# Optimization experiments

Hardware: AMD Instinct MI355X
Metric: run time of the kernel (lower is better)

## Reference

```python
import jax, jax.numpy as jnp
import numpy as np

N_NODES = 200000
N_EDGES = 440000
N_GRAPHS = 4096
EMB = 300
N_LAYERS = 5
TEMP = 0.04
NUM_ATOM_TYPE, NUM_CHIRALITY = 120, 3
NUM_BOND_TYPE, NUM_BOND_DIR = 6, 3
SELF_LOOP_TYPE = 4  # pretrain-gnns convention: self-loop edge_attr = [4, 0]


def setup_inputs() -> dict:
    key = jax.random.key(0)
    ks = jax.random.split(key, 24)
    inp = {}
    for i in (0, 1):
        inp[f"x{i}"] = jax.random.randint(ks[i * 4 + 0], (N_NODES, 2), 0, 3)
        inp[f"edge_index{i}"] = jax.random.randint(ks[i * 4 + 1], (2, N_EDGES), 0, N_NODES)
        inp[f"edge_attr{i}"] = jax.random.randint(ks[i * 4 + 2], (N_EDGES, 2), 0, 3)
        inp[f"batch_ids{i}"] = jnp.sort(jax.random.randint(ks[i * 4 + 3], (N_NODES,), 0, N_GRAPHS))

    def rn(k, shape, s=0.1):
        return (jax.random.normal(k, shape, jnp.float32) * s)

    inp["atom_emb1"] = rn(ks[8], (NUM_ATOM_TYPE, EMB))
    inp["atom_emb2"] = rn(ks[9], (NUM_CHIRALITY, EMB))
    inp["edge_emb1"] = rn(ks[10], (N_LAYERS, NUM_BOND_TYPE, EMB))
    inp["edge_emb2"] = rn(ks[11], (N_LAYERS, NUM_BOND_DIR, EMB))
    inp["W1"] = rn(ks[12], (N_LAYERS, EMB, 2 * EMB))
    inp["bm1"] = jnp.zeros((N_LAYERS, 2 * EMB), jnp.float32)
    inp["W2"] = rn(ks[13], (N_LAYERS, 2 * EMB, EMB))
    inp["bm2"] = jnp.zeros((N_LAYERS, EMB), jnp.float32)
    inp["gamma"] = jnp.ones((N_LAYERS, EMB), jnp.float32)
    inp["beta"] = jnp.zeros((N_LAYERS, EMB), jnp.float32)
    inp["Wp1"] = rn(ks[14], (EMB, EMB))
    inp["bp1"] = jnp.zeros((EMB,), jnp.float32)
    inp["Wp2"] = rn(ks[15], (EMB, EMB))
    inp["bp2"] = jnp.zeros((EMB,), jnp.float32)
    return inp


def _encode(x, edge_index, edge_attr, batch_ids,
            atom_emb1, atom_emb2, edge_emb1, edge_emb2,
            W1, bm1, W2, bm2, gamma, beta, Wp1, bp1, Wp2, bp2):
    n = x.shape[0]
    src, dst = edge_index[0], edge_index[1]
    h = atom_emb1[x[:, 0]] + atom_emb2[x[:, 1]]  # [N, EMB]
    for l in range(N_LAYERS):
        e = edge_emb1[l][edge_attr[:, 0]] + edge_emb2[l][edge_attr[:, 1]]  # [E, EMB]
        self_e = edge_emb1[l][SELF_LOOP_TYPE] + edge_emb2[l][0]  # self-loop edge emb
        # GIN sum aggregation (incl. self-loop message h_i + self_e)
        agg = jax.ops.segment_sum(h[src] + e, dst, num_segments=n) + h + self_e
        h = jax.nn.relu(agg @ W1[l] + bm1[l]) @ W2[l] + bm2[l]
        # BatchNorm over nodes (training-mode statistics, eps=1e-5)
        mean = h.mean(axis=0)
        var = h.var(axis=0)
        h = (h - mean) * jax.lax.rsqrt(var + 1e-5) * gamma[l] + beta[l]
        if l < N_LAYERS - 1:
            h = jax.nn.relu(h)
    # global_mean_pool
    s = jax.ops.segment_sum(h, batch_ids, num_segments=N_GRAPHS)
    c = jax.ops.segment_sum(jnp.ones((n, 1), h.dtype), batch_ids, num_segments=N_GRAPHS)
    g = s / jnp.maximum(c, 1.0)
    out = jax.nn.relu(g @ Wp1 + bp1) @ Wp2 + bp2
    return out / jnp.linalg.norm(out, axis=1, keepdims=True)


def reference(x0, edge_index0, edge_attr0, batch_ids0,
              x1, edge_index1, edge_attr1, batch_ids1,
              atom_emb1, atom_emb2, edge_emb1, edge_emb2,
              W1, bm1, W2, bm2, gamma, beta, Wp1, bp1, Wp2, bp2):
    params = (atom_emb1, atom_emb2, edge_emb1, edge_emb2,
              W1, bm1, W2, bm2, gamma, beta, Wp1, bp1, Wp2, bp2)
    f0 = _encode(x0, edge_index0, edge_attr0, batch_ids0, *params)
    f1 = _encode(x1, edge_index1, edge_attr1, batch_ids1, *params)
    logits = (f0 @ f1.T) / TEMP
    labels = jnp.arange(logits.shape[0])
    return logits, labels
```

## Files before the change

kernel.cpp:

```cpp
#include <hip/hip_runtime.h>
#include <hip/hip_bf16.h>
#include <hip/hip_fp16.h>

#define EMB 300
#define NHID 600
#define NLAYERS 5
#define NG 4096
#define NCOMBO 18
#define SELFCB 12
#define HS 304
#define KP1 320
#define KP2 640
#define SCB 2048

__device__ __forceinline__ void atomAddF(float* p, float v) { unsafeAtomicAdd(p, v); }

struct f8 { unsigned char v; };

__device__ __forceinline__ unsigned char enc8(float x) {
    unsigned xb = __float_as_uint(x);
    unsigned s = (xb >> 24) & 0x80u;
    float a = __uint_as_float(xb & 0x7FFFFFFFu);
    if (!(a < 448.f)) return (unsigned char)(s | 0x7E);
    if (a < 0.0009765625f) return (unsigned char)s;
    if (a < 0.015625f) {
        int m = (int)(a * 512.f + 0.5f);
        if (m > 7) return (unsigned char)(s | 0x08);
        return (unsigned char)(s | (unsigned)m);
    }
    unsigned u = __float_as_uint(a) + 0x80000u;
    int e = (int)(u >> 23) - 127;
    if (e > 8) return (unsigned char)(s | 0x7E);
    unsigned m = (u >> 20) & 7u;
    return (unsigned char)(s | ((unsigned)(e + 7) << 3) | m);
}
__device__ __forceinline__ float dec8(unsigned char c) {
    unsigned s = c & 0x80u, e = (c >> 3) & 0xFu, m = c & 7u;
    float v = (e == 0) ? (float)m * 0.001953125f
                       : __uint_as_float(((e + 120u) << 23) | (m << 20));
    return s ? -v : v;
}

typedef float fx2 __attribute__((ext_vector_type(2)));

#if defined(__has_builtin)
#if __has_builtin(__builtin_amdgcn_cvt_pk_f32_fp8) && __has_builtin(__builtin_amdgcn_cvt_pk_fp8_f32)
#define HWFP8 1
#endif
#endif

__device__ __forceinline__ void dec4(unsigned w, float& v0, float& v1, float& v2, float& v3) {
#ifdef HWFP8
    fx2 lo = __builtin_amdgcn_cvt_pk_f32_fp8((int)w, false);
    fx2 hi = __builtin_amdgcn_cvt_pk_f32_fp8((int)w, true);
    v0 = lo.x; v1 = lo.y; v2 = hi.x; v3 = hi.y;
#else
    v0 = dec8(w & 0xff); v1 = dec8((w >> 8) & 0xff);
    v2 = dec8((w >> 16) & 0xff); v3 = dec8((w >> 24) & 0xff);
#endif
}
__device__ __forceinline__ unsigned enc4(float v0, float v1, float v2, float v3) {
#ifdef HWFP8
    int w = __builtin_amdgcn_cvt_pk_fp8_f32(v0, v1, 0, false);
    w = __builtin_amdgcn_cvt_pk_fp8_f32(v2, v3, w, true);
    return (unsigned)w;
#else
    return (unsigned)enc8(v0) | ((unsigned)enc8(v1) << 8)
         | ((unsigned)enc8(v2) << 16) | ((unsigned)enc8(v3) << 24);
#endif
}
__device__ __forceinline__ unsigned char enc1(float v) {
#ifdef HWFP8
    return (unsigned char)(__builtin_amdgcn_cvt_pk_fp8_f32(v, 0.f, 0, false) & 0xff);
#else
    return enc8(v);
#endif
}
__device__ __forceinline__ float dec1(unsigned char c) {
#ifdef HWFP8
    fx2 lo = __builtin_amdgcn_cvt_pk_f32_fp8((int)(unsigned)c, false);
    return lo.x;
#else
    return dec8(c);
#endif
}

typedef _Float16 f16t;
typedef _Float16 f16x8 __attribute__((ext_vector_type(8)));
typedef float f32x4 __attribute__((ext_vector_type(4)));

__device__ __forceinline__ void stF(float* p, float v) { *p = v; }
__device__ __forceinline__ void stF(__half* p, float v) { *p = __float2half(v); }


__global__ void zero_f32_v6(float* __restrict__ p, long n) {
    long s = (long)gridDim.x * blockDim.x;
    for (long i = blockIdx.x * (long)blockDim.x + threadIdx.x; i < n; i += s) p[i] = 0.f;
}
__global__ void zero_i32_v8(int* __restrict__ p, int n) {
    int s = gridDim.x * blockDim.x;
    for (int i = blockIdx.x * blockDim.x + threadIdx.x; i < n; i += s) p[i] = 0;
}
__global__ void copy_i32_v8(const int* __restrict__ a, int* __restrict__ b, int n) {
    int s = gridDim.x * blockDim.x;
    for (int i = blockIdx.x * blockDim.x + threadIdx.x; i < n; i += s) b[i] = a[i];
}
__global__ void labels_v6(float* __restrict__ out, int n) {
    int i = blockIdx.x * blockDim.x + threadIdx.x;
    if (i < n) out[i] = (float)i;
}


__global__ void hist_dst_v8(const int* __restrict__ ei, int* __restrict__ deg, int E) {
    int s = gridDim.x * blockDim.x;
    for (int e = blockIdx.x * blockDim.x + threadIdx.x; e < E; e += s)
        atomicAdd(&deg[ei[E + e]], 1);
}
__global__ void hist_b_v8(const int* __restrict__ b, int* __restrict__ deg, int n) {
    int s = gridDim.x * blockDim.x;
    for (int i = blockIdx.x * blockDim.x + threadIdx.x; i < n; i += s)
        atomicAdd(&deg[b[i]], 1);
}

__global__ __launch_bounds__(256) void scan_excl_v8(const int* __restrict__ in,
                                                    int* __restrict__ out, int n) {
    __shared__ int part[256];
    int span = (n + 255) / 256;
    int t = threadIdx.x;
    int s0 = t * span, s1 = min(s0 + span, n);
    int sum = 0;
    for (int i = s0; i < s1; ++i) sum += in[i];
    part[t] = sum;
    __syncthreads();
    int v = sum;
    for (int off = 1; off < 256; off <<= 1) {
        int u = (t >= off) ? part[t - off] : 0;
        __syncthreads();
        part[t] += u;
        __syncthreads();
    }
    int run = part[t] - v;
    for (int i = s0; i < s1; ++i) { out[i] = run; run += in[i]; }
    if (t == 255) out[n] = run;
}

__global__ __launch_bounds__(256) void scan_bsum_v10(const int* __restrict__ in,
                                                     int* __restrict__ bsum, int n) {
    __shared__ int red[256];
    int b = blockIdx.x, t = threadIdx.x;
    int base = b * SCB + t * 8;
    int s = 0;
#pragma unroll
    for (int i = 0; i < 8; ++i) { int idx = base + i; if (idx < n) s += in[idx]; }
    red[t] = s; __syncthreads();
#pragma unroll
    for (int o = 128; o > 0; o >>= 1) {
        if (t < o) red[t] += red[t + o];
        __syncthreads();
    }
    if (t == 0) bsum[b] = red[0];
}

__global__ __launch_bounds__(256) void scan_top_v10(int* __restrict__ bsum, int nb,
                                                    int* __restrict__ total_out) {
    __shared__ int part[256];
    int t = threadIdx.x;
    int v = (t < nb) ? bsum[t] : 0;
    part[t] = v;
    __syncthreads();
    for (int o = 1; o < 256; o <<= 1) {
        int u = (t >= o) ? part[t - o] : 0;
        __syncthreads();
        part[t] += u;
        __syncthreads();
    }
    if (t < nb) bsum[t] = part[t] - v;
    if (t == 255) *total_out = part[255];
}

__global__ __launch_bounds__(256) void scan_fill_v10(const int* __restrict__ in,
                                                     const int* __restrict__ bsum,
                                                     int* __restrict__ out, int n) {
    __shared__ int red[256];
    int b = blockIdx.x, t = threadIdx.x;
    int base = b * SCB + t * 8;
    int v[8]; int s = 0;
#pragma unroll
    for (int i = 0; i < 8; ++i) { int idx = base + i; v[i] = (idx < n) ? in[idx] : 0; s += v[i]; }
    red[t] = s;
    __syncthreads();
    int self = s;
    for (int o = 1; o < 256; o <<= 1) {
        int u = (t >= o) ? red[t - o] : 0;
        __syncthreads();
        red[t] += u;
        __syncthreads();
    }
    int run = bsum[b] + red[t] - self;
#pragma unroll
    for (int i = 0; i < 8; ++i) { int idx = base + i; if (idx < n) out[idx] = run; run += v[i]; }
}

__global__ void fill_csr_v8(const int* __restrict__ ei, const int* __restrict__ ea,
                            int* __restrict__ cursor, int* __restrict__ csrc,
                            int* __restrict__ ccombo, int E) {
    int s = gridDim.x * blockDim.x;
    for (int e = blockIdx.x * blockDim.x + threadIdx.x; e < E; e += s) {
        int dst = ei[E + e];
        int pos = atomicAdd(&cursor[dst], 1);
        csrc[pos] = ei[e];
        ccombo[pos] = ea[2 * e] * 3 + ea[2 * e + 1];
    }
}

__global__ void tbl_v8(const float* __restrict__ ee1, const float* __restrict__ ee2,
                       float* __restrict__ tbl) {
    int idx = blockIdx.x * blockDim.x + threadIdx.x;
    if (idx >= NLAYERS * NCOMBO * EMB) return;
    int j = idx % EMB;
    int cb = (idx / EMB) % NCOMBO;
    int l = idx / (EMB * NCOMBO);
    tbl[idx] = ee1[(l * 6 + cb / 3) * EMB + j] + ee2[(l * 3 + cb % 3) * EMB + j];
}

__global__ void wtrans_v9(const float* __restrict__ W, f16t* __restrict__ Wt,
                          int K, int N, int Kpad) {
    int idx = blockIdx.x * blockDim.x + threadIdx.x;
    if (idx >= N * Kpad) return;
    int n = idx / Kpad, k = idx - n * Kpad;
    Wt[idx] = (k < K) ? (f16t)W[(size_t)k * N + n] : (f16t)0.f;
}

__global__ void wtrans8_v13(const float* __restrict__ W, unsigned char* __restrict__ Wt,
                            int K, int N, int Kpad) {
    int idx = blockIdx.x * blockDim.x + threadIdx.x;
    if (idx >= N * Kpad) return;
    int n = idx / Kpad, k = idx - n * Kpad;
    Wt[idx] = (k < K) ? enc8(W[(size_t)k * N + n]) : 0;
}


__global__ void init_h_v11(const int* __restrict__ x, const float* __restrict__ ae1,
                           const float* __restrict__ ae2, unsigned char* __restrict__ h,
                           int N) {
    int s = gridDim.x * blockDim.x;
    int total = N * (HS / 4);
    for (int idx = blockIdx.x * blockDim.x + threadIdx.x; idx < total; idx += s) {
        int i = idx / (HS / 4), d = idx - i * (HS / 4);
        int j = d * 4;
        int x0 = x[2 * i] * EMB, x1 = x[2 * i + 1] * EMB;
        unsigned out = 0;
#pragma unroll
        for (int t = 0; t < 4; ++t) {
            int jj = j + t;
            unsigned char b = 0;
            if (jj < EMB) b = enc8(ae1[x0 + jj] + ae2[x1 + jj]);
            out |= (unsigned)b << (8 * t);
        }
        *(unsigned*)(h + (size_t)i * HS + j) = out;
    }
}

template<bool BN>
__global__ __launch_bounds__(256)
void gather_v18(const unsigned char* __restrict__ h, const int* __restrict__ rp,
                const int* __restrict__ csrc, const int* __restrict__ ccombo,
                const float* __restrict__ tbl, const float* __restrict__ scl,
                const float* __restrict__ sft, unsigned char* __restrict__ aggc,
                int c0, int c1) {
    __shared__ float T[NCOMBO * EMB];
    __shared__ float SC[EMB + 4];
    __shared__ float SF[EMB + 4];
    for (int t = threadIdx.x; t < NCOMBO * EMB; t += 256) T[t] = tbl[t];
    if (BN) {
        for (int t = threadIdx.x; t < EMB; t += 256) { SC[t] = scl[t]; SF[t] = sft[t]; }
    }
    __syncthreads();
    int wid = (blockIdx.x * blockDim.x + threadIdx.x) >> 6;
    int lane = threadIdx.x & 63;
    int nw = (gridDim.x * blockDim.x) >> 6;
    const int jt = 256 + lane;
    float4 sc4, sf4; float sct = 1.f, sff = 0.f;
    if (BN) {
        sc4 = *(const float4*)&SC[lane << 2];
        sf4 = *(const float4*)&SF[lane << 2];
        if (lane < 44) { sct = SC[jt]; sff = SF[jt]; }
    }
#define BNAPP(val, sc, sf) { if (BN) (val) = fmaxf(fmaf((val), (sc), (sf)), 0.f); }
    for (int i = c0 + wid; i < c1; i += nw) {
        int p0 = rp[i], p1 = rp[i + 1];
        float a0, a1, a2, a3, at = 0.f;
        {
            const unsigned char* hr = h + (size_t)i * HS;
            unsigned w = *(const unsigned*)(hr + (lane << 2));
            float4 t4 = *(const float4*)&T[SELFCB * EMB + (lane << 2)];
            float v0, v1, v2, v3;
            dec4(w, v0, v1, v2, v3);
            BNAPP(v0, sc4.x, sf4.x); BNAPP(v1, sc4.y, sf4.y);
            BNAPP(v2, sc4.z, sf4.z); BNAPP(v3, sc4.w, sf4.w);
            a0 = v0 + t4.x; a1 = v1 + t4.y; a2 = v2 + t4.z; a3 = v3 + t4.w;
            if (lane < 44) {
                float vt = dec1(hr[jt]);
                BNAPP(vt, sct, sff);
                at = vt + T[SELFCB * EMB + jt];
            }
        }
        int p = p0;
        for (; p + 1 < p1; p += 2) {
            int sA = csrc[p],     cbA = ccombo[p];
            int sB = csrc[p + 1], cbB = ccombo[p + 1];
            const unsigned char* hA = h + (size_t)sA * HS;
            const unsigned char* hB = h + (size_t)sB * HS;
            unsigned wA = *(const unsigned*)(hA + (lane << 2));
            unsigned wB = *(const unsigned*)(hB + (lane << 2));
            float tA = 0.f, tB = 0.f;
            if (lane < 44) { tA = dec1(hA[jt]); tB = dec1(hB[jt]); }
            {
                float4 t4 = *(const float4*)&T[cbA * EMB + (lane << 2)];
                float v0, v1, v2, v3;
                dec4(wA, v0, v1, v2, v3);
                BNAPP(v0, sc4.x, sf4.x); BNAPP(v1, sc4.y, sf4.y);
                BNAPP(v2, sc4.z, sf4.z); BNAPP(v3, sc4.w, sf4.w);
                a0 += v0 + t4.x; a1 += v1 + t4.y; a2 += v2 + t4.z; a3 += v3 + t4.w;
                if (lane < 44) {
                    BNAPP(tA, sct, sff);
                    at += tA + T[cbA * EMB + jt];
                }
            }
            {
                float4 t4 = *(const float4*)&T[cbB * EMB + (lane << 2)];
                float v0, v1, v2, v3;
                dec4(wB, v0, v1, v2, v3);
                BNAPP(v0, sc4.x, sf4.x); BNAPP(v1, sc4.y, sf4.y);
                BNAPP(v2, sc4.z, sf4.z); BNAPP(v3, sc4.w, sf4.w);
                a0 += v0 + t4.x; a1 += v1 + t4.y; a2 += v2 + t4.z; a3 += v3 + t4.w;
                if (lane < 44) {
                    BNAPP(tB, sct, sff);
                    at += tB + T[cbB * EMB + jt];
                }
            }
        }
        if (p < p1) {
            int sA = csrc[p], cbA = ccombo[p];
            const unsigned char* hA = h + (size_t)sA * HS;
            unsigned wA = *(const unsigned*)(hA + (lane << 2));
            float4 t4 = *(const float4*)&T[cbA * EMB + (lane << 2)];
            float v0, v1, v2, v3;
            dec4(wA, v0, v1, v2, v3);
            BNAPP(v0, sc4.x, sf4.x); BNAPP(v1, sc4.y, sf4.y);
            BNAPP(v2, sc4.z, sf4.z); BNAPP(v3, sc4.w, sf4.w);
            a0 += v0 + t4.x; a1 += v1 + t4.y; a2 += v2 + t4.z; a3 += v3 + t4.w;
            if (lane < 44) {
                float vt = dec1(hA[jt]);
                BNAPP(vt, sct, sff);
                at += vt + T[cbA * EMB + jt];
            }
        }
        unsigned char* out = aggc + (size_t)(i - c0) * KP1;
        *(unsigned*)(out + (lane << 2)) = enc4(a0, a1, a2, a3);
        if (lane < 44) out[jt] = enc1(at);
    }
#undef BNAPP
}

template<int MODE, bool STATS>
__global__ __launch_bounds__(256)
void fast_gemm8_v16(const unsigned char* __restrict__ A, int lda,
                    const unsigned char* __restrict__ Bt, int ldb,
                    const float* __restrict__ bias, unsigned char* __restrict__ C,
                    int ldc, int M, int N, int Kpad, int gx,
                    float* __restrict__ sums)
{
    __shared__ char smem[26624];
    char* AlB = smem;
    char* BlB = smem + 9216;
    const int tid = threadIdx.x;
    const int lane = tid & 63;
    const int wid = tid >> 6;
    const int wr = (wid >> 1) << 6;
    const int wc = (wid & 1) << 6;

    const int nwg = gridDim.x;
    const int q = nwg >> 3, r = nwg & 7;
    const int xcd = blockIdx.x & 7, idx = blockIdx.x >> 3;
    const int swz = (xcd < r ? xcd * (q + 1) : r * (q + 1) + (xcd - r) * q) + idx;
    const int row0 = (swz / gx) * 128;
    const int col0 = (swz % gx) * 128;

    f32x4 acc[4][4] = {};
    const int nkt = Kpad >> 6;
    const int sr = tid >> 1;
    const int skb = (tid & 1) << 5;

    for (int kt = 0; kt < nkt; ++kt) {
        const int k0 = kt << 6;
        {
            const int gr = row0 + sr;
            const unsigned char* src = A + (size_t)gr * lda + k0 + skb;
            int4 v0 = {0, 0, 0, 0}, v1 = {0, 0, 0, 0};
            if (gr < M) { v0 = *(const int4*)src; v1 = *(const int4*)(src + 16); }
            char* dst = AlB + sr * 72 + skb;
            *(long*)(dst)      = ((const long*)&v0)[0];
            *(long*)(dst + 8)  = ((const long*)&v0)[1];
            *(long*)(dst + 16) = ((const long*)&v1)[0];
            *(long*)(dst + 24) = ((const long*)&v1)[1];
        }
        {
            const int gc = col0 + sr;
            const unsigned char* src = Bt + (size_t)gc * ldb + k0 + skb;
            int4 v0 = {0, 0, 0, 0}, v1 = {0, 0, 0, 0};
            if (gc < N) { v0 = *(const int4*)src; v1 = *(const int4*)(src + 16); }
            char* dst = BlB + sr * 72 + skb;
            *(long*)(dst)      = ((const long*)&v0)[0];
            *(long*)(dst + 8)  = ((const long*)&v0)[1];
            *(long*)(dst + 16) = ((const long*)&v1)[0];
            *(long*)(dst + 24) = ((const long*)&v1)[1];
        }
        __syncthreads();
        const int fr = lane & 15;
        const int kbase = (lane >> 4) << 3;
#pragma unroll
        for (int ks = 0; ks < 2; ++ks) {
            const int kg = kbase + ks * 32;
            long af[4], bf[4];
#pragma unroll
            for (int mi = 0; mi < 4; ++mi)
                af[mi] = *(const long*)(AlB + (wr + mi * 16 + fr) * 72 + kg);
#pragma unroll
            for (int ni = 0; ni < 4; ++ni)
                bf[ni] = *(const long*)(BlB + (wc + ni * 16 + fr) * 72 + kg);
#pragma unroll
            for (int mi = 0; mi < 4; ++mi)
#pragma unroll
                for (int ni = 0; ni < 4; ++ni)
                    acc[mi][ni] = __builtin_amdgcn_mfma_f32_16x16x32_fp8_fp8(
                        af[mi], bf[ni], acc[mi][ni], 0, 0, 0);
        }
        __syncthreads();
    }
    char* Cl = smem;
    float* Sred = (float*)(smem + 18432);
    float* Qred = (float*)(smem + 22528);
    const int fr = lane & 15;
    const int rb = (lane >> 4) << 2;
    const int slot = ((wid >> 1) << 2) | (lane >> 4);
#pragma unroll
    for (int ni = 0; ni < 4; ++ni) {
        const int cb = wc + ni * 16 + fr;
        const int c = col0 + cb;
        const float bv = (c < N) ? bias[c] : 0.f;
        float lsum = 0.f, lsq = 0.f;
#pragma unroll
        for (int mi = 0; mi < 4; ++mi) {
#pragma unroll
            for (int i = 0; i < 4; ++i) {
                const int rloc = wr + mi * 16 + rb + i;
                float v = acc[mi][ni][i] + bv;
                if (MODE == 2) v = fmaxf(v, 0.f);
                Cl[rloc * 144 + cb] = (char)enc1(v);
                if (STATS && (row0 + rloc) < M && c < N) {
                    lsum += v; lsq = fmaf(v, v, lsq);
                }
            }
        }
        if (STATS) { Sred[cb * 8 + slot] = lsum; Qred[cb * 8 + slot] = lsq; }
    }
    __syncthreads();
    {
        const int rloc = tid >> 1;
        const int half = (tid & 1) << 6;
        const int grow = row0 + rloc;
        if (grow < M) {
            int cmax = ldc - col0; if (cmax > 128) cmax = 128;
            unsigned char* dst = C + (size_t)grow * ldc + col0;
            const char* srcl = Cl + rloc * 144 + half;
#pragma unroll
            for (int qi = 0; qi < 4; ++qi) {
                if (half + qi * 16 + 16 <= cmax)
                    *(int4*)(dst + half + qi * 16) = *(const int4*)(srcl + qi * 16);
            }
        }
    }
    if (STATS) {
        if (tid < 128) {
            const int c = col0 + tid;
            if (c < N) {
                float s = 0.f, qq = 0.f;
#pragma unroll
                for (int k = 0; k < 8; ++k) { s += Sred[tid * 8 + k]; qq += Qred[tid * 8 + k]; }
                atomAddF(&sums[c], s);
                atomAddF(&sums[EMB + c], qq);
            }
        }
    }
}

template<typename TO, int MODE>
__global__ __launch_bounds__(256)
void fast_gemm_v12(const f16t* __restrict__ A, int lda,
                   const f16t* __restrict__ Bt, int ldb,
                   const float* __restrict__ bias, TO* __restrict__ C, int ldc,
                   int M, int N, int Kpad, float scale)
{
    __shared__ f16t Al[128][76];
    __shared__ f16t Bl[128][76];
    const int tid = threadIdx.x;
    const int lane = tid & 63;
    const int wid = tid >> 6;
    const int wr = (wid >> 1) << 6;
    const int wc = (wid & 1) << 6;
    const int row0 = blockIdx.y * 128;
    const int col0 = blockIdx.x * 128;
    f32x4 acc[4][4] = {};
    const int nkt = Kpad >> 6;
    const int sr = tid >> 1;
    const int skb = (tid & 1) << 5;

    for (int kt = 0; kt < nkt; ++kt) {
        const int k0 = kt << 6;
        {
            const int gr = row0 + sr;
            const f16t* src = A + (size_t)gr * lda + k0 + skb;
            f16x8 v0 = {}, v1 = {}, v2 = {}, v3 = {};
            if (gr < M) {
                v0 = *(const f16x8*)(src);
                v1 = *(const f16x8*)(src + 8);
                v2 = *(const f16x8*)(src + 16);
                v3 = *(const f16x8*)(src + 24);
            }
            *(f16x8*)&Al[sr][skb]      = v0;
            *(f16x8*)&Al[sr][skb + 8]  = v1;
            *(f16x8*)&Al[sr][skb + 16] = v2;
            *(f16x8*)&Al[sr][skb + 24] = v3;
        }
        {
            const int gc = col0 + sr;
            const f16t* src = Bt + (size_t)gc * ldb + k0 + skb;
            f16x8 v0 = {}, v1 = {}, v2 = {}, v3 = {};
            if (gc < N) {
                v0 = *(const f16x8*)(src);
                v1 = *(const f16x8*)(src + 8);
                v2 = *(const f16x8*)(src + 16);
                v3 = *(const f16x8*)(src + 24);
            }
            *(f16x8*)&Bl[sr][skb]      = v0;
            *(f16x8*)&Bl[sr][skb + 8]  = v1;
            *(f16x8*)&Bl[sr][skb + 16] = v2;
            *(f16x8*)&Bl[sr][skb + 24] = v3;
        }
        __syncthreads();
        const int fr = lane & 15;
        const int kbase = (lane >> 4) << 3;
#pragma unroll
        for (int ks = 0; ks < 2; ++ks) {
            const int kg8 = kbase + ks * 32;
            f16x8 af[4], bf[4];
#pragma unroll
            for (int mi = 0; mi < 4; ++mi)
                af[mi] = *(const f16x8*)&Al[wr + mi * 16 + fr][kg8];
#pragma unroll
            for (int ni = 0; ni < 4; ++ni)
                bf[ni] = *(const f16x8*)&Bl[wc + ni * 16 + fr][kg8];
#pragma unroll
            for (int mi = 0; mi < 4; ++mi)
#pragma unroll
                for (int ni = 0; ni < 4; ++ni)
                    acc[mi][ni] = __builtin_amdgcn_mfma_f32_16x16x32_f16(
                        af[mi], bf[ni], acc[mi][ni], 0, 0, 0);
        }
        __syncthreads();
    }
    const int fr = lane & 15;
    const int rb = (lane >> 4) << 2;
#pragma unroll
    for (int ni = 0; ni < 4; ++ni) {
        const int c = col0 + wc + ni * 16 + fr;
        if (c >= N) continue;
        const float bv = (MODE == 1 || MODE == 2) ? bias[c] : 0.f;
#pragma unroll
        for (int mi = 0; mi < 4; ++mi) {
#pragma unroll
            for (int i = 0; i < 4; ++i) {
                const int r = row0 + wr + mi * 16 + rb + i;
                if (r >= M) continue;
                float v = acc[mi][ni][i];
                if (MODE == 1 || MODE == 2) v += bv;
                if (MODE == 2) v = fmaxf(v, 0.f);
                v *= scale;
                if (MODE == 3) v = fmaxf(-26.f, fminf(26.f, v));
                stF(&C[(size_t)r * ldc + c], v);
            }
        }
    }
}


__global__ void bn_finalize_v6(const float* __restrict__ sums,
                               const float* __restrict__ gamma, const float* __restrict__ beta,
                               float* __restrict__ scl, float* __restrict__ sft, float inv_n) {
    int j = threadIdx.x;
    if (j < EMB) {
        float m = sums[j] * inv_n;
        float var = sums[EMB + j] * inv_n - m * m;
        float sc = gamma[j] * rsqrtf(var + 1e-5f);
        scl[j] = sc;
        sft[j] = beta[j] - m * sc;
    }
}


__global__ __launch_bounds__(256) void pool_seg_v11(const unsigned char* __restrict__ h,
                                                    const int* __restrict__ gptr,
                                                    const float* __restrict__ scl,
                                                    const float* __restrict__ sft,
                                                    __half* __restrict__ poolh) {
    int g = blockIdx.x;
    int s0 = gptr[g], s1 = gptr[g + 1];
    float inv = (s1 > s0) ? 1.f / (float)(s1 - s0) : 0.f;
    for (int j = threadIdx.x; j < EMB; j += 256) {
        float s = 0.f;
        for (int r = s0; r < s1; ++r) s += dec1(h[(size_t)r * HS + j]);
        float mv = (s1 > s0) ? fmaf(s * inv, scl[j], sft[j]) : 0.f;
        poolh[(size_t)g * KP1 + j] = __float2half(mv);
    }
}


__global__ __launch_bounds__(256) void rownorm_f16_v12(const float* __restrict__ f,
                                                       f16t* __restrict__ fh) {
    __shared__ float red[256];
    __shared__ float inv;
    int r = blockIdx.x, tid = threadIdx.x;
    const float* row = f + (size_t)r * EMB;
    float s = 0.f;
    for (int j = tid; j < EMB; j += 256) { float v = row[j]; s = fmaf(v, v, s); }
    red[tid] = s;
    __syncthreads();
#pragma unroll
    for (int o = 128; o > 0; o >>= 1) {
        if (tid < o) red[tid] += red[tid + o];
        __syncthreads();
    }
    if (tid == 0) inv = rsqrtf(fmaxf(red[0], 1e-30f));
    __syncthreads();
    float iv = inv;
    for (int j = tid; j < KP1; j += 256)
        fh[(size_t)r * KP1 + j] = (j < EMB) ? (f16t)(row[j] * iv) : (f16t)0.f;
}


extern "C" void kernel_launch(void* const* d_in, const int* in_sizes, int n_in,
                              void* d_out, int out_size, void* d_ws, size_t ws_size,
                              hipStream_t stream) {
    const int N = in_sizes[0] / 2;
    const int E = in_sizes[1] / 2;

    const float* atom1 = (const float*)d_in[8];
    const float* atom2 = (const float*)d_in[9];
    const float* ee1   = (const float*)d_in[10];
    const float* ee2   = (const float*)d_in[11];
    const float* W1    = (const float*)d_in[12];
    const float* bm1   = (const float*)d_in[13];
    const float* W2    = (const float*)d_in[14];
    const float* bm2   = (const float*)d_in[15];
    const float* gamma = (const float*)d_in[16];
    const float* beta  = (const float*)d_in[17];
    const float* Wp1   = (const float*)d_in[18];
    const float* bp1   = (const float*)d_in[19];
    const float* Wp2   = (const float*)d_in[20];
    const float* bp2   = (const float*)d_in[21];

    float* ob = (float*)d_out;

    unsigned char* h0 = (unsigned char*)d_out;
    bool h0_fits = ((size_t)N * HS) <= ((size_t)NG * NG * 4 - 256);

    size_t off = 0;
    char* base = (char*)d_ws;
    auto take = [&](size_t bytes) -> char* {
        char* p = base + off;
        off += (bytes + 255) & ~(size_t)255;
        return p;
    };
    unsigned char* h1 = (unsigned char*)take((size_t)N * HS);
    float* fbuf   = (float*)take((size_t)NG * EMB * 4);
    f16t*  fh     = (f16t*)take((size_t)2 * NG * KP1 * 2);
    float* sums   = (float*)take(2 * EMB * 4);
    float* scl    = (float*)take((size_t)NLAYERS * EMB * 4);
    float* sft    = (float*)take((size_t)NLAYERS * EMB * 4);
    int*   deg    = (int*)take((size_t)N * 4);
    int*   rp     = (int*)take((size_t)(N + 1) * 4);
    int*   cursor = (int*)take((size_t)N * 4);
    int*   csrc   = (int*)take((size_t)E * 4);
    int*   ccombo = (int*)take((size_t)E * 4);
    int*   bsum   = (int*)take(256 * 4);
    int*   gdeg   = (int*)take((size_t)NG * 4);
    int*   gptr   = (int*)take((size_t)(NG + 1) * 4);
    float* tbl    = (float*)take((size_t)NLAYERS * NCOMBO * EMB * 4);
    unsigned char* W1t8 = (unsigned char*)take((size_t)NLAYERS * NHID * KP1);
    unsigned char* W2t8 = (unsigned char*)take((size_t)NLAYERS * EMB * KP2);
    f16t*  Wp1t   = (f16t*)take((size_t)EMB * KP1 * 2);
    f16t*  Wp2t   = (f16t*)take((size_t)EMB * KP1 * 2);
    __half* poolh = (__half*)take((size_t)NG * KP1 * 2);
    __half* p1h   = (__half*)take((size_t)NG * KP1 * 2);

    long CN = 0;
    if (h0_fits && ws_size > off + 1024) {
        CN = (long)((ws_size - off - 1024) / (KP1 + KP2));
        if (CN > N) CN = N;
    }
    if (CN < 1024) {
        zero_f32_v6<<<2048, 256, 0, stream>>>(ob, (long)NG * NG);
        labels_v6<<<(NG + 255) / 256, 256, 0, stream>>>(ob + (size_t)NG * NG, NG);
        return;
    }
    unsigned char* aggc = (unsigned char*)take((size_t)CN * KP1);
    unsigned char* z    = (unsigned char*)take((size_t)CN * KP2);

    tbl_v8<<<(NLAYERS * NCOMBO * EMB + 255) / 256, 256, 0, stream>>>(ee1, ee2, tbl);
    for (int l = 0; l < NLAYERS; ++l) {
        wtrans8_v13<<<(NHID * KP1 + 255) / 256, 256, 0, stream>>>(
            W1 + (size_t)l * EMB * NHID, W1t8 + (size_t)l * NHID * KP1, EMB, NHID, KP1);
        wtrans8_v13<<<(EMB * KP2 + 255) / 256, 256, 0, stream>>>(
            W2 + (size_t)l * NHID * EMB, W2t8 + (size_t)l * EMB * KP2, NHID, EMB, KP2);
    }
    wtrans_v9<<<(EMB * KP1 + 255) / 256, 256, 0, stream>>>(Wp1, Wp1t, EMB, EMB, KP1);
    wtrans_v9<<<(EMB * KP1 + 255) / 256, 256, 0, stream>>>(Wp2, Wp2t, EMB, EMB, KP1);
    zero_f32_v6<<<2048, 256, 0, stream>>>((float*)aggc, CN * (KP1 / 4));
    zero_f32_v6<<<2048, 256, 0, stream>>>((float*)z, CN * (KP2 / 4));
    zero_f32_v6<<<1024, 256, 0, stream>>>((float*)poolh, (long)NG * (KP1 / 2));
    zero_f32_v6<<<1024, 256, 0, stream>>>((float*)p1h, (long)NG * (KP1 / 2));

    const int nb = (N + SCB - 1) / SCB;

    for (int enc = 0; enc < 2; ++enc) {
        const int* x  = (const int*)d_in[enc * 4 + 0];
        const int* ei = (const int*)d_in[enc * 4 + 1];
        const int* ea = (const int*)d_in[enc * 4 + 2];
        const int* bi = (const int*)d_in[enc * 4 + 3];

        zero_i32_v8<<<256, 256, 0, stream>>>(deg, N);
        hist_dst_v8<<<1024, 256, 0, stream>>>(ei, deg, E);
        scan_bsum_v10<<<nb, 256, 0, stream>>>(deg, bsum, N);
        scan_top_v10<<<1, 256, 0, stream>>>(bsum, nb, rp + N);
        scan_fill_v10<<<nb, 256, 0, stream>>>(deg, bsum, rp, N);
        copy_i32_v8<<<256, 256, 0, stream>>>(rp, cursor, N);
        fill_csr_v8<<<1024, 256, 0, stream>>>(ei, ea, cursor, csrc, ccombo, E);
        zero_i32_v8<<<64, 256, 0, stream>>>(gdeg, NG);
        hist_b_v8<<<1024, 256, 0, stream>>>(bi, gdeg, N);
        scan_excl_v8<<<1, 256, 0, stream>>>(gdeg, gptr, NG);

        unsigned char* hc = h0;
        unsigned char* hn = h1;
        init_h_v11<<<4096, 256, 0, stream>>>(x, atom1, atom2, hc, N);

        for (int l = 0; l < NLAYERS; ++l) {
            const unsigned char* W1l = W1t8 + (size_t)l * NHID * KP1;
            const unsigned char* W2l = W2t8 + (size_t)l * EMB * KP2;
            const float* tl = tbl + (size_t)l * NCOMBO * EMB;
            const float* scp = scl + (size_t)(l - 1) * EMB;
            const float* sfp = sft + (size_t)(l - 1) * EMB;

            zero_f32_v6<<<1, 1024, 0, stream>>>(sums, 2 * EMB);

            for (long c0 = 0; c0 < N; c0 += CN) {
                int m = (int)((N - c0 < CN) ? (N - c0) : CN);
                if (l == 0)
                    gather_v18<false><<<2048, 256, 0, stream>>>(
                        hc, rp, csrc, ccombo, tl, nullptr, nullptr,
                        aggc, (int)c0, (int)(c0 + m));
                else
                    gather_v18<true><<<2048, 256, 0, stream>>>(
                        hc, rp, csrc, ccombo, tl, scp, sfp,
                        aggc, (int)c0, (int)(c0 + m));
                int gx1 = (NHID + 127) / 128, gy1 = (m + 127) / 128;
                fast_gemm8_v16<2, false><<<gx1 * gy1, 256, 0, stream>>>(
                    aggc, KP1, W1l, KP1, bm1 + l * NHID,
                    z, KP2, m, NHID, KP1, gx1, nullptr);
                int gx2 = (EMB + 127) / 128;
                fast_gemm8_v16<1, true><<<gx2 * gy1, 256, 0, stream>>>(
                    z, KP2, W2l, KP2, bm2 + l * EMB,
                    hn + (size_t)c0 * HS, HS, m, EMB, KP2, gx2, sums);
            }

            bn_finalize_v6<<<1, 320, 0, stream>>>(sums, gamma + l * EMB, beta + l * EMB,
                                                  scl + (size_t)l * EMB,
                                                  sft + (size_t)l * EMB, 1.f / (float)N);
            unsigned char* t = hc; hc = hn; hn = t;
        }

        pool_seg_v11<<<NG, 256, 0, stream>>>(hc, gptr,
                                             scl + (size_t)(NLAYERS - 1) * EMB,
                                             sft + (size_t)(NLAYERS - 1) * EMB, poolh);

        dim3 gp((EMB + 127) / 128, (NG + 127) / 128);
        fast_gemm_v12<__half, 2><<<gp, 256, 0, stream>>>(
            (const f16t*)poolh, KP1, Wp1t, KP1, bp1, p1h, KP1, NG, EMB, KP1, 1.f);
        fast_gemm_v12<float, 1><<<gp, 256, 0, stream>>>(
            (const f16t*)p1h, KP1, Wp2t, KP1, bp2, fbuf, EMB, NG, EMB, KP1, 1.f);
        rownorm_f16_v12<<<NG, 256, 0, stream>>>(fbuf, fh + (size_t)enc * NG * KP1);
    }

    f16t* f0h = fh;
    f16t* f1h = fh + (size_t)NG * KP1;
    dim3 gl(NG / 128, NG / 128);
    fast_gemm_v12<float, 3><<<gl, 256, 0, stream>>>(
        f0h, KP1, f1h, KP1, nullptr, ob, NG, NG, NG, KP1, 25.f);
    labels_v6<<<(NG + 255) / 256, 256, 0, stream>>>(ob + (size_t)NG * NG, NG);
}
```

Baseline: 4.328 ms.

## Fuse the two FP8 MLP GEMMs into one kernel keeping the hidden tile in LDS

Replaces the two separate FP8 GEMM launches (agg→z with ReLU, z→h with BN stats) with one fused kernel per 64-row tile. The 64×640 hidden activation is kept in shared memory instead of being written to and read back from a global z buffer, which also frees workspace so the chunk size can grow. The cost is a 55KB LDS footprint per block that limits occupancy, smaller 64-row tiles, and W1/W2 being reloaded for every row tile. Row blocks no longer use the XCD swizzle.

```diff
diff --git a/kernel.cpp b/kernel.cpp
--- a/kernel.cpp
+++ b/kernel.cpp
@@ -14,8 +14,6 @@
 #define SCB 2048
 
 __device__ __forceinline__ void atomAddF(float* p, float v) { unsafeAtomicAdd(p, v); }
-
-struct f8 { unsigned char v; };
 
 __device__ __forceinline__ unsigned char enc8(float x) {
     unsigned xb = __float_as_uint(x);
@@ -363,135 +361,192 @@
 #undef BNAPP
 }
 
-template<int MODE, bool STATS>
 __global__ __launch_bounds__(256)
-void fast_gemm8_v16(const unsigned char* __restrict__ A, int lda,
-                    const unsigned char* __restrict__ Bt, int ldb,
-                    const float* __restrict__ bias, unsigned char* __restrict__ C,
-                    int ldc, int M, int N, int Kpad, int gx,
-                    float* __restrict__ sums)
+void fused_mlp_v19(const unsigned char* __restrict__ A,
+                   const unsigned char* __restrict__ W1t, const float* __restrict__ b1,
+                   const unsigned char* __restrict__ W2t, const float* __restrict__ b2,
+                   unsigned char* __restrict__ H, int ldh, int M,
+                   float* __restrict__ sums)
 {
-    __shared__ char smem[26624];
-    char* AlB = smem;
-    char* BlB = smem + 9216;
+    __shared__ char smem[55296];
+    char* Ast = smem;
+    char* Bst = smem + 4608;
+    char* zL  = smem + 13824;
     const int tid = threadIdx.x;
     const int lane = tid & 63;
-    const int wid = tid >> 6;
-    const int wr = (wid >> 1) << 6;
-    const int wc = (wid & 1) << 6;
-
-    const int nwg = gridDim.x;
-    const int q = nwg >> 3, r = nwg & 7;
-    const int xcd = blockIdx.x & 7, idx = blockIdx.x >> 3;
-    const int swz = (xcd < r ? xcd * (q + 1) : r * (q + 1) + (xcd - r) * q) + idx;
-    const int row0 = (swz / gx) * 128;
-    const int col0 = (swz % gx) * 128;
-
-    f32x4 acc[4][4] = {};
-    const int nkt = Kpad >> 6;
-    const int sr = tid >> 1;
-    const int skb = (tid & 1) << 5;
-
-    for (int kt = 0; kt < nkt; ++kt) {
-        const int k0 = kt << 6;
-        {
-            const int gr = row0 + sr;
-            const unsigned char* src = A + (size_t)gr * lda + k0 + skb;
-            int4 v0 = {0, 0, 0, 0}, v1 = {0, 0, 0, 0};
-            if (gr < M) { v0 = *(const int4*)src; v1 = *(const int4*)(src + 16); }
-            char* dst = AlB + sr * 72 + skb;
-            *(long*)(dst)      = ((const long*)&v0)[0];
-            *(long*)(dst + 8)  = ((const long*)&v0)[1];
-            *(long*)(dst + 16) = ((const long*)&v1)[0];
-            *(long*)(dst + 24) = ((const long*)&v1)[1];
-        }
-        {
-            const int gc = col0 + sr;
-            const unsigned char* src = Bt + (size_t)gc * ldb + k0 + skb;
-            int4 v0 = {0, 0, 0, 0}, v1 = {0, 0, 0, 0};
-            if (gc < N) { v0 = *(const int4*)src; v1 = *(const int4*)(src + 16); }
-            char* dst = BlB + sr * 72 + skb;
-            *(long*)(dst)      = ((const long*)&v0)[0];
-            *(long*)(dst + 8)  = ((const long*)&v0)[1];
-            *(long*)(dst + 16) = ((const long*)&v1)[0];
-            *(long*)(dst + 24) = ((const long*)&v1)[1];
-        }
-        __syncthreads();
-        const int fr = lane & 15;
-        const int kbase = (lane >> 4) << 3;
-#pragma unroll
-        for (int ks = 0; ks < 2; ++ks) {
-            const int kg = kbase + ks * 32;
-            long af[4], bf[4];
+    const int wgid = tid >> 6;
+    const int wc = wgid << 5;
+    const int row0 = blockIdx.x * 64;
+    const int fr = lane & 15;
+    const int kbase = (lane >> 4) << 3;
+    const int rb = (lane >> 4) << 2;
+
+    for (int nc = 0; nc < 5; ++nc) {
+        f32x4 acc[4][2] = {};
+        for (int kt = 0; kt < 5; ++kt) {
+            const int k0 = kt << 6;
+            {
+                int r = tid >> 2, sg = (tid & 3) << 4;
+                int4 v = {0, 0, 0, 0};
+                int gr = row0 + r;
+                if (gr < M) v = *(const int4*)(A + (size_t)gr * KP1 + k0 + sg);
+                char* d = Ast + r * 72 + sg;
+                *(long*)(d)     = ((const long*)&v)[0];
+                *(long*)(d + 8) = ((const long*)&v)[1];
+            }
+            {
+                int c = tid >> 1, sg = (tid & 1) << 5;
+                int gc = nc * 128 + c;
+                int4 v0 = {0, 0, 0, 0}, v1 = {0, 0, 0, 0};
+                if (gc < NHID) {
+                    const unsigned char* src = W1t + (size_t)gc * KP1 + k0 + sg;
+                    v0 = *(const int4*)src; v1 = *(const int4*)(src + 16);
+                }
+                char* d = Bst + c * 72 + sg;
+                *(long*)(d)      = ((const long*)&v0)[0];
+                *(long*)(d + 8)  = ((const long*)&v0)[1];
+                *(long*)(d + 16) = ((const long*)&v1)[0];
+                *(long*)(d + 24) = ((const long*)&v1)[1];
+            }
+            __syncthreads();
+#pragma unroll
+            for (int ks = 0; ks < 2; ++ks) {
+                const int kg = kbase + ks * 32;
+                long af[4], bf[2];
+#pragma unroll
+                for (int mi = 0; mi < 4; ++mi)
+                    af[mi] = *(const long*)(Ast + (mi * 16 + fr) * 72 + kg);
+#pragma unroll
+                for (int ni = 0; ni < 2; ++ni)
+                    bf[ni] = *(const long*)(Bst + (wc + ni * 16 + fr) * 72 + kg);
+#pragma unroll
+                for (int mi = 0; mi < 4; ++mi)
+#pragma unroll
+                    for (int ni = 0; ni < 2; ++ni)
+                        acc[mi][ni] = __builtin_amdgcn_mfma_f32_16x16x32_fp8_fp8(
+                            af[mi], bf[ni], acc[mi][ni], 0, 0, 0);
+            }
+            __syncthreads();
+        }
+#pragma unroll
+        for (int ni = 0; ni < 2; ++ni) {
+            const int zc = nc * 128 + wc + ni * 16 + fr;
+            const float bv = (zc < NHID) ? b1[zc] : 0.f;
 #pragma unroll
             for (int mi = 0; mi < 4; ++mi)
-                af[mi] = *(const long*)(AlB + (wr + mi * 16 + fr) * 72 + kg);
-#pragma unroll
-            for (int ni = 0; ni < 4; ++ni)
-                bf[ni] = *(const long*)(BlB + (wc + ni * 16 + fr) * 72 + kg);
+#pragma unroll
+                for (int i = 0; i < 4; ++i) {
+                    const int rloc = mi * 16 + rb + i;
+                    float v = fmaxf(acc[mi][ni][i] + bv, 0.f);
+                    zL[rloc * 648 + zc] = (char)enc1(v);
+                }
+        }
+        __syncthreads();
+    }
+
+    char* Cl = Ast;
+    float* Sred = (float*)Bst;
+    float* Qred = (float*)(Bst + 2048);
+    for (int nc = 0; nc < 3; ++nc) {
+        const int col0 = nc * 128;
+        f32x4 acc[4][2] = {};
+        for (int kt = 0; kt < 10; ++kt) {
+            const int k0 = kt << 6;
+            {
+                int c = tid >> 1, sg = (tid & 1) << 5;
+                int gc = col0 + c;
+                int4 v0 = {0, 0, 0, 0}, v1 = {0, 0, 0, 0};
+                if (gc < EMB) {
+                    const unsigned char* src = W2t + (size_t)gc * KP2 + k0 + sg;
+                    v0 = *(const int4*)src; v1 = *(const int4*)(src + 16);
+                }
+                char* d = Bst + c * 72 + sg;
+                *(long*)(d)      = ((const long*)&v0)[0];
+                *(long*)(d + 8)  = ((const long*)&v0)[1];
+                *(long*)(d + 16) = ((const long*)&v1)[0];
+                *(long*)(d + 24) = ((const long*)&v1)[1];
+            }
+            __syncthreads();
+#pragma unroll
+            for (int ks = 0; ks < 2; ++ks) {
+                const int kgz = k0 + kbase + ks * 32;
+                const int kgb = kbase + ks * 32;
+                long af[4], bf[2];
+#pragma unroll
+                for (int mi = 0; mi < 4; ++mi)
+                    af[mi] = *(const long*)(zL + (mi * 16 + fr) * 648 + kgz);
+#pragma unroll
+                for (int ni = 0; ni < 2; ++ni)
+                    bf[ni] = *(const long*)(Bst + (wc + ni * 16 + fr) * 72 + kgb);
+#pragma unroll
+                for (int mi = 0; mi < 4; ++mi)
+#pragma unroll
+                    for (int ni = 0; ni < 2; ++ni)
+                        acc[mi][ni] = __builtin_amdgcn_mfma_f32_16x16x32_fp8_fp8(
+                            af[mi], bf[ni], acc[mi][ni], 0, 0, 0);
+            }
+            __syncthreads();
+        }
+#pragma unroll
+        for (int ni = 0; ni < 2; ++ni) {
+            const int cb = wc + ni * 16 + fr;
+            const int c = col0 + cb;
+            const float bv = (c < EMB) ? b2[c] : 0.f;
+            float ls = 0.f, lq = 0.f;
 #pragma unroll
             for (int mi = 0; mi < 4; ++mi)
 #pragma unroll
-                for (int ni = 0; ni < 4; ++ni)
-                    acc[mi][ni] = __builtin_amdgcn_mfma_f32_16x16x32_fp8_fp8(
-                        af[mi], bf[ni], acc[mi][ni], 0, 0, 0);
-        }
-        __syncthreads();
-    }
-    char* Cl = smem;
-    float* Sred = (float*)(smem + 18432);
-    float* Qred = (float*)(smem + 22528);
-    const int fr = lane & 15;
-    const int rb = (lane >> 4) << 2;
-    const int slot = ((wid >> 1) << 2) | (lane >> 4);
-#pragma unroll
-    for (int ni = 0; ni < 4; ++ni) {
-        const int cb = wc + ni * 16 + fr;
-        const int c = col0 + cb;
-        const float bv = (c < N) ? bias[c] : 0.f;
-        float lsum = 0.f, lsq = 0.f;
-#pragma unroll
-        for (int mi = 0; mi < 4; ++mi) {
-#pragma unroll
-            for (int i = 0; i < 4; ++i) {
-                const int rloc = wr + mi * 16 + rb + i;
-                float v = acc[mi][ni][i] + bv;
-                if (MODE == 2) v = fmaxf(v, 0.f);
-                Cl[rloc * 144 + cb] = (char)enc1(v);
-                if (STATS && (row0 + rloc) < M && c < N) {
-                    lsum += v; lsq = fmaf(v, v, lsq);
+                for (int i = 0; i < 4; ++i) {
+                    const int rloc = mi * 16 + rb + i;
+                    if (row0 + rloc < M && c < EMB) {
+                        float v = acc[mi][ni][i] + bv;
+                        ls += v; lq = fmaf(v, v, lq);
+                    }
                 }
-            }
-        }
-        if (STATS) { Sred[cb * 8 + slot] = lsum; Qred[cb * 8 + slot] = lsq; }
-    }
-    __syncthreads();
-    {
-        const int rloc = tid >> 1;
-        const int half = (tid & 1) << 6;
-        const int grow = row0 + rloc;
-        if (grow < M) {
-            int cmax = ldc - col0; if (cmax > 128) cmax = 128;
-            unsigned char* dst = C + (size_t)grow * ldc + col0;
-            const char* srcl = Cl + rloc * 144 + half;
-#pragma unroll
-            for (int qi = 0; qi < 4; ++qi) {
-                if (half + qi * 16 + 16 <= cmax)
-                    *(int4*)(dst + half + qi * 16) = *(const int4*)(srcl + qi * 16);
-            }
-        }
-    }
-    if (STATS) {
+            Sred[cb * 4 + (lane >> 4)] = ls;
+            Qred[cb * 4 + (lane >> 4)] = lq;
+        }
+        __syncthreads();
         if (tid < 128) {
-            const int c = col0 + tid;
-            if (c < N) {
-                float s = 0.f, qq = 0.f;
-#pragma unroll
-                for (int k = 0; k < 8; ++k) { s += Sred[tid * 8 + k]; qq += Qred[tid * 8 + k]; }
+            int c = col0 + tid;
+            if (c < EMB) {
+                float s = Sred[tid * 4] + Sred[tid * 4 + 1]
+                        + Sred[tid * 4 + 2] + Sred[tid * 4 + 3];
+                float q = Qred[tid * 4] + Qred[tid * 4 + 1]
+                        + Qred[tid * 4 + 2] + Qred[tid * 4 + 3];
                 atomAddF(&sums[c], s);
-                atomAddF(&sums[EMB + c], qq);
-            }
-        }
+                atomAddF(&sums[EMB + c], q);
+            }
+        }
+        for (int hp = 0; hp < 2; ++hp) {
+            __syncthreads();
+            if ((wgid >> 1) == hp) {
+#pragma unroll
+                for (int ni = 0; ni < 2; ++ni) {
+                    const int lc = wc + ni * 16 + fr - hp * 64;
+                    const int c = col0 + wc + ni * 16 + fr;
+                    const float bv = (c < EMB) ? b2[c] : 0.f;
+#pragma unroll
+                    for (int mi = 0; mi < 4; ++mi)
+#pragma unroll
+                        for (int i = 0; i < 4; ++i) {
+                            const int rloc = mi * 16 + rb + i;
+                            float v = (c < EMB) ? (acc[mi][ni][i] + bv) : 0.f;
+                            Cl[rloc * 72 + lc] = (char)enc1(v);
+                        }
+                }
+            }
+            __syncthreads();
+            {
+                int r = tid >> 2, sg = (tid & 3) << 4;
+                int grow = row0 + r;
+                int gcol = col0 + hp * 64 + sg;
+                if (grow < M && gcol + 16 <= ldh) {
+                    *(int4*)(H + (size_t)grow * ldh + gcol) = *(const int4*)(Cl + r * 72 + sg);
+                }
+            }
+        }
+        __syncthreads();
     }
 }
 
@@ -706,7 +761,7 @@
 
     long CN = 0;
     if (h0_fits && ws_size > off + 1024) {
-        CN = (long)((ws_size - off - 1024) / (KP1 + KP2));
+        CN = (long)((ws_size - off - 1024) / KP1);
         if (CN > N) CN = N;
     }
     if (CN < 1024) {
@@ -715,7 +770,6 @@
         return;
     }
     unsigned char* aggc = (unsigned char*)take((size_t)CN * KP1);
-    unsigned char* z    = (unsigned char*)take((size_t)CN * KP2);
 
     tbl_v8<<<(NLAYERS * NCOMBO * EMB + 255) / 256, 256, 0, stream>>>(ee1, ee2, tbl);
     for (int l = 0; l < NLAYERS; ++l) {
@@ -727,7 +781,6 @@
     wtrans_v9<<<(EMB * KP1 + 255) / 256, 256, 0, stream>>>(Wp1, Wp1t, EMB, EMB, KP1);
     wtrans_v9<<<(EMB * KP1 + 255) / 256, 256, 0, stream>>>(Wp2, Wp2t, EMB, EMB, KP1);
     zero_f32_v6<<<2048, 256, 0, stream>>>((float*)aggc, CN * (KP1 / 4));
-    zero_f32_v6<<<2048, 256, 0, stream>>>((float*)z, CN * (KP2 / 4));
     zero_f32_v6<<<1024, 256, 0, stream>>>((float*)poolh, (long)NG * (KP1 / 2));
     zero_f32_v6<<<1024, 256, 0, stream>>>((float*)p1h, (long)NG * (KP1 / 2));
 
@@ -773,14 +826,10 @@
                     gather_v18<true><<<2048, 256, 0, stream>>>(
                         hc, rp, csrc, ccombo, tl, scp, sfp,
                         aggc, (int)c0, (int)(c0 + m));
-                int gx1 = (NHID + 127) / 128, gy1 = (m + 127) / 128;
-                fast_gemm8_v16<2, false><<<gx1 * gy1, 256, 0, stream>>>(
-                    aggc, KP1, W1l, KP1, bm1 + l * NHID,
-                    z, KP2, m, NHID, KP1, gx1, nullptr);
-                int gx2 = (EMB + 127) / 128;
-                fast_gemm8_v16<1, true><<<gx2 * gy1, 256, 0, stream>>>(
-                    z, KP2, W2l, KP2, bm2 + l * EMB,
-                    hn + (size_t)c0 * HS, HS, m, EMB, KP2, gx2, sums);
+                int gy = (m + 63) / 64;
+                fused_mlp_v19<<<gy, 256, 0, stream>>>(
+                    aggc, W1l, bm1 + l * NHID, W2l, bm2 + l * EMB,
+                    hn + (size_t)c0 * HS, HS, m, sums);
             }
 
             bn_finalize_v6<<<1, 320, 0, stream>>>(sums, gamma + l * EMB, beta + l * EMB,
```

Result: slower. 5.048 ms (median of 2 runs) (+16.6%).
